# Kernel tuning notes

Hardware: AMD Instinct MI355X
Metric: run time of the kernel (lower is better)

The kernel has to match this reference:

```python
import jax, jax.numpy as jnp
import numpy as np

N_NODES = 50000
N_EDGES = 800000
IN_DIM = 64
EDGE_DIM = 16
HID = 128
L = 3
G = 128  # number of graphs in the batch
EPS = 1e-5


def _glorot(key, shape):
    fan_in, fan_out = shape[0], shape[1]
    lim = float(np.sqrt(6.0 / (fan_in + fan_out)))
    return jax.random.uniform(key, shape, jnp.float32, -lim, lim)


def setup_inputs() -> dict:
    key = jax.random.key(0)
    ks = jax.random.split(key, 40)
    inp = {}
    inp["x"] = jax.random.uniform(ks[0], (N_NODES, IN_DIM), jnp.float32)
    inp["edge_index"] = jax.random.randint(ks[1], (2, N_EDGES), 0, N_NODES, jnp.int64)
    inp["edge_attr"] = jax.random.normal(ks[2], (N_EDGES, EDGE_DIM), jnp.float32)
    inp["batch"] = jnp.sort(jax.random.randint(ks[3], (N_NODES,), 0, G, jnp.int64))
    # ligand / protein input MLPs: Linear-ReLU-Linear-ReLU
    inp["lig_w1"] = _glorot(ks[4], (IN_DIM, HID)); inp["lig_b1"] = jnp.zeros((HID,), jnp.float32)
    inp["lig_w2"] = _glorot(ks[5], (HID, HID));    inp["lig_b2"] = jnp.zeros((HID,), jnp.float32)
    inp["prot_w1"] = _glorot(ks[6], (IN_DIM, HID)); inp["prot_b1"] = jnp.zeros((HID,), jnp.float32)
    inp["prot_w2"] = _glorot(ks[7], (HID, HID));    inp["prot_b2"] = jnp.zeros((HID,), jnp.float32)
    # per-layer GINEConv params (stacked over layers)
    inp["edge_w"] = jnp.stack([_glorot(ks[8 + i], (EDGE_DIM, HID)) for i in range(L)])
    inp["edge_b"] = jnp.zeros((L, HID), jnp.float32)
    inp["nn_w1"] = jnp.stack([_glorot(ks[12 + i], (HID, HID)) for i in range(L)])
    inp["nn_b1"] = jnp.zeros((L, HID), jnp.float32)
    inp["nn_w2"] = jnp.stack([_glorot(ks[16 + i], (HID, HID)) for i in range(L)])
    inp["nn_b2"] = jnp.zeros((L, HID), jnp.float32)
    # GraphNorm params: weight=1, bias=0, mean_scale=1
    inp["gn_w"] = jnp.ones((L, HID), jnp.float32)
    inp["gn_b"] = jnp.zeros((L, HID), jnp.float32)
    inp["gn_ms"] = jnp.ones((L, HID), jnp.float32)
    # output head: Linear-ReLU-Linear(1)
    inp["fc_w1"] = _glorot(ks[20], (HID, HID)); inp["fc_b1"] = jnp.zeros((HID,), jnp.float32)
    inp["fc_w2"] = _glorot(ks[21], (HID, 1));   inp["fc_b2"] = jnp.zeros((1,), jnp.float32)
    return inp


def reference(x, edge_index, edge_attr, batch,
              lig_w1, lig_b1, lig_w2, lig_b2,
              prot_w1, prot_b1, prot_w2, prot_b2,
              edge_w, edge_b, nn_w1, nn_b1, nn_w2, nn_b2,
              gn_w, gn_b, gn_ms,
              fc_w1, fc_b1, fc_w2, fc_b2):
    relu = lambda a: jnp.maximum(a, 0)
    src, dst = edge_index[0], edge_index[1]

    # input encoders, merged per node by protein flag (last feature column)
    is_prot = x[:, -1] > 0.5
    h_lig = relu(relu(x @ lig_w1 + lig_b1) @ lig_w2 + lig_b2)
    h_prot = relu(relu(x @ prot_w1 + prot_b1) @ prot_w2 + prot_b2)
    h = jnp.where(is_prot[:, None], h_prot, h_lig)

    # per-graph node counts for GraphNorm
    cnt = jax.ops.segment_sum(jnp.ones((x.shape[0],), jnp.float32), batch, num_segments=G)
    cnt = jnp.maximum(cnt, 1.0)[:, None]

    for l in range(L):
        # GINEConv (eps=0): out = nn(x + sum_{j->i} relu(x_j + lin(e_ji)))
        e = edge_attr @ edge_w[l] + edge_b[l]              # [E, HID]
        msg = relu(h[src] + e)                             # gather + add + relu
        aggr = jax.ops.segment_sum(msg, dst, num_segments=h.shape[0])
        h = aggr + h
        h = relu(h @ nn_w1[l] + nn_b1[l]) @ nn_w2[l] + nn_b2[l]
        # GraphNorm: per-graph mean/var with learnable mean_scale
        mean = jax.ops.segment_sum(h, batch, num_segments=G) / cnt
        hc = h - mean[batch] * gn_ms[l]
        var = jax.ops.segment_sum(hc * hc, batch, num_segments=G) / cnt
        h = gn_w[l] * hc * jax.lax.rsqrt(var[batch] + EPS) + gn_b[l]
        h = relu(h)  # (dropout=0.0 -> identity)

    g = jax.ops.segment_sum(h, batch, num_segments=G)      # global_add_pool
    out = relu(g @ fc_w1 + fc_b1) @ fc_w2 + fc_b2
    return out.reshape(-1)
```

## Files before the change

### kernel.cpp

```cpp
#include <hip/hip_runtime.h>

#define N_NODES 50000
#define N_EDGES 800000
#define IN_DIM  64
#define EDGE_DIM 16
#define HID     128
#define NLAYERS 3
#define NGRAPH  128
#define EPS     1e-5f

typedef __attribute__((ext_vector_type(8))) short bf8_t;
typedef __attribute__((ext_vector_type(4))) float f32x4;

__device__ __forceinline__ unsigned short f2bf(float x) {
    unsigned u = __float_as_uint(x);
    unsigned r = u + 0x7fffu + ((u >> 16) & 1u);
    return (unsigned short)(r >> 16);
}
__device__ __forceinline__ float bf2f(unsigned short v) {
    return __uint_as_float(((unsigned)v) << 16);
}

__global__ void k_init(int* __restrict__ row_cnt, float* __restrict__ pool,
                       float* __restrict__ gsum, float* __restrict__ gsq) {
    int i = blockIdx.x * blockDim.x + threadIdx.x;
    if (i < N_NODES) row_cnt[i] = 0;
    if (i < NGRAPH * HID) { pool[i] = 0.0f; gsum[i] = 0.0f; gsq[i] = 0.0f; }
}

__global__ __launch_bounds__(NGRAPH) void k_count(const int* __restrict__ batch,
                                                  float* __restrict__ cnt) {
    int g = threadIdx.x;
    int lo = 0, hi = N_NODES;
    while (lo < hi) { int mid = (lo + hi) >> 1; if (batch[mid] < g) lo = mid + 1; else hi = mid; }
    int a = lo;
    lo = 0; hi = N_NODES;
    while (lo < hi) { int mid = (lo + hi) >> 1; if (batch[mid] < g + 1) lo = mid + 1; else hi = mid; }
    cnt[g] = (float)(lo - a);
}

__global__ void k_wconv(const float* __restrict__ nw1, const float* __restrict__ nw2,
                        unsigned short* __restrict__ wt) {
    int idx = blockIdx.x * 256 + threadIdx.x;
    if (idx >= NLAYERS * 2 * HID * HID) return;
    int k = idx & 127;
    int n = (idx >> 7) & 127;
    int which = (idx >> 14) & 1;
    int l = idx >> 15;
    const float* w = (which == 0 ? nw1 : nw2) + l * HID * HID;
    wt[idx] = f2bf(w[k * HID + n]);
}

__global__ void k_wconv_enc(const float* __restrict__ lw1, const float* __restrict__ pw1,
                            const float* __restrict__ lw2, const float* __restrict__ pw2,
                            unsigned short* __restrict__ we) {
    int idx = blockIdx.x * 256 + threadIdx.x;
    if (idx >= 49152) return;
    float v;
    if (idx < 8192)       { int n = idx >> 6, k = idx & 63;            v = lw1[k * HID + n]; }
    else if (idx < 16384) { int r = idx - 8192;  int n = r >> 6, k = r & 63;  v = pw1[k * HID + n]; }
    else if (idx < 32768) { int r = idx - 16384; int n = r >> 7, k = r & 127; v = lw2[k * HID + n]; }
    else                  { int r = idx - 32768; int n = r >> 7, k = r & 127; v = pw2[k * HID + n]; }
    we[idx] = f2bf(v);
}

__global__ void k_wconv_e(const float* __restrict__ ew, unsigned short* __restrict__ wte) {
    int idx = blockIdx.x * 256 + threadIdx.x;
    if (idx >= NLAYERS * 8 * 64 * 8) return;
    int j = idx & 7;
    int lane = (idx >> 3) & 63;
    int t = (idx >> 9) & 7;
    int l = idx >> 12;
    int k = (lane >> 4) * 8 + j;
    int feat = t * 16 + (lane & 15);
    float v = (k < EDGE_DIM) ? ew[l * EDGE_DIM * HID + k * HID + feat] : 0.0f;
    wte[idx] = f2bf(v);
}

__global__ void k_hist(const int* __restrict__ dsts, int* __restrict__ row_cnt) {
    int e = blockIdx.x * blockDim.x + threadIdx.x;
    if (e < N_EDGES) atomicAdd(&row_cnt[dsts[e]], 1);
}

__global__ __launch_bounds__(256) void k_scan1(const int* __restrict__ row_cnt,
                                               int* __restrict__ partial) {
    __shared__ int s[256];
    int t = threadIdx.x, b = blockIdx.x;
    int i0 = b * 512 + t;
    int v = 0;
    if (i0 < N_NODES) v += row_cnt[i0];
    if (i0 + 256 < N_NODES) v += row_cnt[i0 + 256];
    s[t] = v; __syncthreads();
    for (int off = 128; off > 0; off >>= 1) {
        if (t < off) s[t] += s[t + off];
        __syncthreads();
    }
    if (t == 0) partial[b] = s[0];
}

#define NCHUNK 98
__global__ __launch_bounds__(128) void k_scan2(int* __restrict__ partial) {
    __shared__ int s[128];
    int t = threadIdx.x;
    int v = (t < NCHUNK) ? partial[t] : 0;
    s[t] = v; __syncthreads();
    for (int off = 1; off < 128; off <<= 1) {
        int x = (t >= off) ? s[t - off] : 0;
        __syncthreads();
        s[t] += x;
        __syncthreads();
    }
    partial[t] = s[t] - v;
}

__global__ __launch_bounds__(512) void k_scan3(const int* __restrict__ row_cnt,
                                               const int* __restrict__ partial,
                                               int* __restrict__ row_start,
                                               int* __restrict__ row_fill) {
    __shared__ int s[512];
    int t = threadIdx.x, b = blockIdx.x;
    int i = b * 512 + t;
    int v = (i < N_NODES) ? row_cnt[i] : 0;
    s[t] = v; __syncthreads();
    for (int off = 1; off < 512; off <<= 1) {
        int x = (t >= off) ? s[t - off] : 0;
        __syncthreads();
        s[t] += x;
        __syncthreads();
    }
    int excl = s[t] - v + partial[b];
    if (i < N_NODES) { row_start[i] = excl; row_fill[i] = excl; }
}

__global__ void k_fill(const int* __restrict__ srcs, const int* __restrict__ dsts,
                       const float* __restrict__ ea,
                       int* __restrict__ row_fill,
                       int* __restrict__ csr_src, unsigned short* __restrict__ cea) {
    int e = blockIdx.x * blockDim.x + threadIdx.x;
    if (e < N_EDGES) {
        int p = atomicAdd(&row_fill[dsts[e]], 1);
        csr_src[p] = srcs[e];
        const float* s = ea + (size_t)e * EDGE_DIM;
        bf8_t v0, v1;
        #pragma unroll
        for (int k = 0; k < 8; ++k) v0[k] = (short)f2bf(s[k]);
        #pragma unroll
        for (int k = 0; k < 8; ++k) v1[k] = (short)f2bf(s[8 + k]);
        *(bf8_t*)(cea + (size_t)p * EDGE_DIM) = v0;
        *(bf8_t*)(cea + (size_t)p * EDGE_DIM + 8) = v1;
    }
}

#define HS 136
__global__ __launch_bounds__(256) void k_encoder_mfma(
    const float* __restrict__ x,
    const unsigned short* __restrict__ we,
    const float* __restrict__ lb1, const float* __restrict__ lb2,
    const float* __restrict__ pb1, const float* __restrict__ pb2,
    unsigned short* __restrict__ Hbp) {
    __shared__ short h1l[4 * 16 * HS];
    __shared__ short h1p[4 * 16 * HS];
    int w = threadIdx.x >> 6, lane = threadIdx.x & 63;
    int m = lane & 15, quad = lane >> 4;
    int nb = blockIdx.x * 64 + w * 16;
    short* hl = h1l + w * 16 * HS;
    short* hp = h1p + w * 16 * HS;
    int nclamp = nb + m; if (nclamp >= N_NODES) nclamp = N_NODES - 1;
    const float* xp = x + (size_t)nclamp * IN_DIM;

    f32x4 a1l[8], a1p[8];
    #pragma unroll
    for (int t = 0; t < 8; ++t) {
        float bl = lb1[t * 16 + m], bp = pb1[t * 16 + m];
        a1l[t] = (f32x4){bl, bl, bl, bl};
        a1p[t] = (f32x4){bp, bp, bp, bp};
    }
    #pragma unroll
    for (int s_ = 0; s_ < 2; ++s_) {
        int k0 = s_ * 32 + quad * 8;
        float4 a0 = *(const float4*)(xp + k0);
        float4 a1v = *(const float4*)(xp + k0 + 4);
        bf8_t af;
        af[0] = (short)f2bf(a0.x); af[1] = (short)f2bf(a0.y);
        af[2] = (short)f2bf(a0.z); af[3] = (short)f2bf(a0.w);
        af[4] = (short)f2bf(a1v.x); af[5] = (short)f2bf(a1v.y);
        af[6] = (short)f2bf(a1v.z); af[7] = (short)f2bf(a1v.w);
        #pragma unroll
        for (int t = 0; t < 8; ++t) {
            bf8_t bl = *(const bf8_t*)(we + (t * 16 + m) * 64 + k0);
            bf8_t bp = *(const bf8_t*)(we + 8192 + (t * 16 + m) * 64 + k0);
            a1l[t] = __builtin_amdgcn_mfma_f32_16x16x32_bf16(af, bl, a1l[t], 0, 0, 0);
            a1p[t] = __builtin_amdgcn_mfma_f32_16x16x32_bf16(af, bp, a1p[t], 0, 0, 0);
        }
    }
    #pragma unroll
    for (int t = 0; t < 8; ++t)
        #pragma unroll
        for (int r = 0; r < 4; ++r) {
            hl[(quad * 4 + r) * HS + t * 16 + m] = (short)f2bf(fmaxf(a1l[t][r], 0.0f));
            hp[(quad * 4 + r) * HS + t * 16 + m] = (short)f2bf(fmaxf(a1p[t][r], 0.0f));
        }
    __syncthreads();
    f32x4 a2l[8], a2p[8];
    #pragma unroll
    for (int t = 0; t < 8; ++t) {
        float bl = lb2[t * 16 + m], bp = pb2[t * 16 + m];
        a2l[t] = (f32x4){bl, bl, bl, bl};
        a2p[t] = (f32x4){bp, bp, bp, bp};
    }
    #pragma unroll
    for (int s_ = 0; s_ < 4; ++s_) {
        int k0 = s_ * 32 + quad * 8;
        bf8_t afl = *(const bf8_t*)(hl + m * HS + k0);
        bf8_t afp = *(const bf8_t*)(hp + m * HS + k0);
        #pragma unroll
        for (int t = 0; t < 8; ++t) {
            bf8_t bl = *(const bf8_t*)(we + 16384 + (t * 16 + m) * 128 + k0);
            bf8_t bp = *(const bf8_t*)(we + 32768 + (t * 16 + m) * 128 + k0);
            a2l[t] = __builtin_amdgcn_mfma_f32_16x16x32_bf16(afl, bl, a2l[t], 0, 0, 0);
            a2p[t] = __builtin_amdgcn_mfma_f32_16x16x32_bf16(afp, bp, a2p[t], 0, 0, 0);
        }
    }
    #pragma unroll
    for (int r = 0; r < 4; ++r) {
        int node = nb + quad * 4 + r;
        if (node < N_NODES) {
            float flg = x[(size_t)node * IN_DIM + (IN_DIM - 1)];
            bool prot = flg > 0.5f;
            bf8_t o;
            #pragma unroll
            for (int t = 0; t < 8; ++t) {
                float v = prot ? a2p[t][r] : a2l[t][r];
                o[t] = (short)f2bf(fmaxf(v, 0.0f));
            }
            *(bf8_t*)(Hbp + (size_t)node * HID + m * 8) = o;
        }
    }
}

__global__ __launch_bounds__(256) void k_gather(
    const int* __restrict__ csr_src, const unsigned short* __restrict__ cea,
    const int* __restrict__ row_start, const int* __restrict__ row_end,
    const unsigned short* __restrict__ wte, const float* __restrict__ eb,
    const unsigned short* __restrict__ Hbp, float* __restrict__ A) {
    int w = threadIdx.x >> 6, lane = threadIdx.x & 63;
    int m = lane & 15, quad = lane >> 4;
    int n = blockIdx.x * 4 + w;
    bf8_t bw[8];
    #pragma unroll
    for (int t = 0; t < 8; ++t)
        bw[t] = *(const bf8_t*)(wte + ((size_t)t * 64 + lane) * 8);
    float ebv[8];
    #pragma unroll
    for (int t = 0; t < 8; ++t) ebv[t] = eb[t * 16 + m];
    float acc[8];
    #pragma unroll
    for (int t = 0; t < 8; ++t) acc[t] = 0.0f;

    int p  = __builtin_amdgcn_readfirstlane(row_start[n]);
    int pe = __builtin_amdgcn_readfirstlane(row_end[n]);

    for (; p + 16 <= pe; p += 16) {
        bf8_t af = (bf8_t){0, 0, 0, 0, 0, 0, 0, 0};
        if (quad < 2)
            af = *(const bf8_t*)(cea + (size_t)(p + m) * EDGE_DIM + quad * 8);
        int sr[4];
        #pragma unroll
        for (int r = 0; r < 4; ++r) sr[r] = csr_src[p + quad * 4 + r];
        bf8_t hrow[4];
        #pragma unroll
        for (int r = 0; r < 4; ++r)
            hrow[r] = *(const bf8_t*)(Hbp + (size_t)sr[r] * HID + m * 8);
        f32x4 d[8];
        #pragma unroll
        for (int t = 0; t < 8; ++t)
            d[t] = __builtin_amdgcn_mfma_f32_16x16x32_bf16(
                af, bw[t], (f32x4){ebv[t], ebv[t], ebv[t], ebv[t]}, 0, 0, 0);
        #pragma unroll
        for (int t = 0; t < 8; ++t)
            #pragma unroll
            for (int r = 0; r < 4; ++r)
                acc[t] += fmaxf(bf2f((unsigned short)hrow[r][t]) + d[t][r], 0.0f);
    }
    int rem = pe - p;
    if (rem > 0) {
        bf8_t af = (bf8_t){0, 0, 0, 0, 0, 0, 0, 0};
        if (quad < 2 && m < rem)
            af = *(const bf8_t*)(cea + (size_t)(p + m) * EDGE_DIM + quad * 8);
        int sr[4];
        #pragma unroll
        for (int r = 0; r < 4; ++r) {
            int idx = p + quad * 4 + r; if (idx >= pe) idx = pe - 1;
            sr[r] = csr_src[idx];
        }
        bf8_t hrow[4];
        #pragma unroll
        for (int r = 0; r < 4; ++r)
            hrow[r] = *(const bf8_t*)(Hbp + (size_t)sr[r] * HID + m * 8);
        f32x4 d[8];
        #pragma unroll
        for (int t = 0; t < 8; ++t)
            d[t] = __builtin_amdgcn_mfma_f32_16x16x32_bf16(
                af, bw[t], (f32x4){ebv[t], ebv[t], ebv[t], ebv[t]}, 0, 0, 0);
        #pragma unroll
        for (int t = 0; t < 8; ++t)
            #pragma unroll
            for (int r = 0; r < 4; ++r)
                if (quad * 4 + r < rem)
                    acc[t] += fmaxf(bf2f((unsigned short)hrow[r][t]) + d[t][r], 0.0f);
    }
    #pragma unroll
    for (int t = 0; t < 8; ++t) {
        acc[t] += __shfl_xor(acc[t], 16);
        acc[t] += __shfl_xor(acc[t], 32);
    }
    int t0 = quad * 2, t1 = quad * 2 + 1;
    const unsigned short* selfp = Hbp + (size_t)n * HID + m * 8;
    float s0 = bf2f(selfp[t0]);
    float s1 = bf2f(selfp[t1]);
    size_t base = (size_t)n * HID;
    A[base + t0 * 16 + m] = acc[t0] + s0;
    A[base + t1 * 16 + m] = acc[t1] + s1;
}

#define MLP_NODES_PER_BLOCK 64
__global__ __launch_bounds__(256) void k_mlp_mfma(
    const float* __restrict__ A, const int* __restrict__ batch,
    const unsigned short* __restrict__ wt1, const unsigned short* __restrict__ wt2,
    const float* __restrict__ b1, const float* __restrict__ b2,
    float* __restrict__ H, float* __restrict__ gsum, float* __restrict__ gsq) {
    __shared__ short h1s[4 * 16 * HS];
    int w = threadIdx.x >> 6;
    int lane = threadIdx.x & 63;
    int m = lane & 15;
    int quad = lane >> 4;
    int nb = blockIdx.x * MLP_NODES_PER_BLOCK + w * 16;
    short* hw = h1s + w * 16 * HS;

    int nclamp = nb + m; if (nclamp >= N_NODES) nclamp = N_NODES - 1;
    const float* Ap = A + (size_t)nclamp * HID;
    f32x4 acc1[8];
    #pragma unroll
    for (int t = 0; t < 8; ++t) {
        float bv = b1[t * 16 + m];
        acc1[t] = (f32x4){bv, bv, bv, bv};
    }
    #pragma unroll
    for (int s_ = 0; s_ < 4; ++s_) {
        int k0 = s_ * 32 + quad * 8;
        float4 a0 = *(const float4*)(Ap + k0);
        float4 a1 = *(const float4*)(Ap + k0 + 4);
        bf8_t af;
        af[0] = (short)f2bf(a0.x); af[1] = (short)f2bf(a0.y);
        af[2] = (short)f2bf(a0.z); af[3] = (short)f2bf(a0.w);
        af[4] = (short)f2bf(a1.x); af[5] = (short)f2bf(a1.y);
        af[6] = (short)f2bf(a1.z); af[7] = (short)f2bf(a1.w);
        #pragma unroll
        for (int t = 0; t < 8; ++t) {
            bf8_t bf = *(const bf8_t*)(wt1 + (t * 16 + m) * HID + k0);
            acc1[t] = __builtin_amdgcn_mfma_f32_16x16x32_bf16(af, bf, acc1[t], 0, 0, 0);
        }
    }
    #pragma unroll
    for (int t = 0; t < 8; ++t)
        #pragma unroll
        for (int r = 0; r < 4; ++r) {
            float v = fmaxf(acc1[t][r], 0.0f);
            hw[(quad * 4 + r) * HS + t * 16 + m] = (short)f2bf(v);
        }
    __syncthreads();
    f32x4 acc2[8];
    #pragma unroll
    for (int t = 0; t < 8; ++t) {
        float bv = b2[t * 16 + m];
        acc2[t] = (f32x4){bv, bv, bv, bv};
    }
    #pragma unroll
    for (int s_ = 0; s_ < 4; ++s_) {
        int k0 = s_ * 32 + quad * 8;
        bf8_t af = *(const bf8_t*)(hw + m * HS + k0);
        #pragma unroll
        for (int t = 0; t < 8; ++t) {
            bf8_t bf = *(const bf8_t*)(wt2 + (t * 16 + m) * HID + k0);
            acc2[t] = __builtin_amdgcn_mfma_f32_16x16x32_bf16(af, bf, acc2[t], 0, 0, 0);
        }
    }
    #pragma unroll
    for (int t = 0; t < 8; ++t)
        #pragma unroll
        for (int r = 0; r < 4; ++r) {
            int node = nb + quad * 4 + r;
            if (node < N_NODES) H[(size_t)node * HID + t * 16 + m] = acc2[t][r];
        }
    int blast = nb + 15 < N_NODES ? batch[nb + 15] : -1;
    int g0 = batch[nb < N_NODES ? nb : N_NODES - 1];
    if (nb + 15 < N_NODES && g0 == blast) {
        #pragma unroll
        for (int t = 0; t < 8; ++t) {
            float s = 0.0f, q = 0.0f;
            #pragma unroll
            for (int r = 0; r < 4; ++r) { float v = acc2[t][r]; s += v; q += v * v; }
            s += __shfl_xor(s, 16); q += __shfl_xor(q, 16);
            s += __shfl_xor(s, 32); q += __shfl_xor(q, 32);
            if (quad == 0) {
                atomicAdd(&gsum[g0 * HID + t * 16 + m], s);
                atomicAdd(&gsq[g0 * HID + t * 16 + m], q);
            }
        }
    } else {
        #pragma unroll
        for (int t = 0; t < 8; ++t)
            #pragma unroll
            for (int r = 0; r < 4; ++r) {
                int node = nb + quad * 4 + r;
                if (node < N_NODES) {
                    int g = batch[node];
                    float v = acc2[t][r];
                    atomicAdd(&gsum[g * HID + t * 16 + m], v);
                    atomicAdd(&gsq[g * HID + t * 16 + m], v * v);
                }
            }
    }
}

__global__ __launch_bounds__(HID) void k_stats(
    float* __restrict__ gsum, float* __restrict__ gsq,
    const float* __restrict__ cnt,
    const float* __restrict__ gw, const float* __restrict__ gb,
    const float* __restrict__ gms,
    float* __restrict__ sc, float* __restrict__ of) {
    int g = blockIdx.x;
    int t = threadIdx.x;
    float c = fmaxf(cnt[g], 1.0f);
    float mean = gsum[g * HID + t] / c;
    float msq  = gsq[g * HID + t] / c;
    float ms = gms[t];
    float var = msq - mean * mean * ms * (2.0f - ms);
    var = fmaxf(var, 0.0f);
    float istd = rsqrtf(var + EPS);
    float s = gw[t] * istd;
    sc[g * HID + t] = s;
    of[g * HID + t] = gb[t] - s * mean * ms;
    gsum[g * HID + t] = 0.0f;
    gsq[g * HID + t]  = 0.0f;
}

#define NORM_N 8
__global__ __launch_bounds__(HID) void k_norm(
    const float* __restrict__ H, const int* __restrict__ batch,
    const float* __restrict__ sc, const float* __restrict__ of,
    unsigned short* __restrict__ Hbp, float* __restrict__ pool, int accumulate) {
    int n0 = blockIdx.x * NORM_N;
    int t = threadIdx.x;
    int m = t & 15, tt = t >> 4;
    int g0 = batch[n0], gN = batch[n0 + NORM_N - 1];
    if (g0 == gN) {
        float ssc = sc[g0 * HID + t], sof = of[g0 * HID + t];
        float ps = 0.0f;
        #pragma unroll
        for (int i = 0; i < NORM_N; ++i) {
            float v = fmaxf(H[(size_t)(n0 + i) * HID + t] * ssc + sof, 0.0f);
            Hbp[(size_t)(n0 + i) * HID + m * 8 + tt] = f2bf(v);
            ps += v;
        }
        if (accumulate) atomicAdd(&pool[g0 * HID + t], ps);
    } else {
        #pragma unroll
        for (int i = 0; i < NORM_N; ++i) {
            int g = batch[n0 + i];
            float v = fmaxf(H[(size_t)(n0 + i) * HID + t] * sc[g * HID + t] + of[g * HID + t], 0.0f);
            Hbp[(size_t)(n0 + i) * HID + m * 8 + tt] = f2bf(v);
            if (accumulate) atomicAdd(&pool[g * HID + t], v);
        }
    }
}

__global__ __launch_bounds__(HID) void k_head(
    const float* __restrict__ pool,
    const float* __restrict__ fw1, const float* __restrict__ fb1,
    const float* __restrict__ fw2, const float* __restrict__ fb2,
    float* __restrict__ out) {
    __shared__ float ps[HID];
    __shared__ float red[2];
    int g = blockIdx.x;
    int t = threadIdx.x;
    ps[t] = pool[g * HID + t];
    __syncthreads();
    float acc = fb1[t];
    #pragma unroll 4
    for (int k = 0; k < HID; ++k) acc = fmaf(ps[k], fw1[k * HID + t], acc);
    float p = fmaxf(acc, 0.0f) * fw2[t];
    #pragma unroll
    for (int off = 32; off > 0; off >>= 1) p += __shfl_down(p, off, 64);
    if ((t & 63) == 0) red[t >> 6] = p;
    __syncthreads();
    if (t == 0) out[g] = red[0] + red[1] + fb2[0];
}

extern "C" void kernel_launch(void* const* d_in, const int* in_sizes, int n_in,
                              void* d_out, int out_size, void* d_ws, size_t ws_size,
                              hipStream_t stream) {
    const float* x     = (const float*)d_in[0];
    const int*   ei    = (const int*)d_in[1];
    const float* ea    = (const float*)d_in[2];
    const int*   batch = (const int*)d_in[3];
    const float* lw1 = (const float*)d_in[4];
    const float* lb1 = (const float*)d_in[5];
    const float* lw2 = (const float*)d_in[6];
    const float* lb2 = (const float*)d_in[7];
    const float* pw1 = (const float*)d_in[8];
    const float* pb1 = (const float*)d_in[9];
    const float* pw2 = (const float*)d_in[10];
    const float* pb2 = (const float*)d_in[11];
    const float* ew  = (const float*)d_in[12];
    const float* eb  = (const float*)d_in[13];
    const float* nw1 = (const float*)d_in[14];
    const float* nb1 = (const float*)d_in[15];
    const float* nw2 = (const float*)d_in[16];
    const float* nb2 = (const float*)d_in[17];
    const float* gw  = (const float*)d_in[18];
    const float* gb  = (const float*)d_in[19];
    const float* gms = (const float*)d_in[20];
    const float* fw1 = (const float*)d_in[21];
    const float* fb1 = (const float*)d_in[22];
    const float* fw2 = (const float*)d_in[23];
    const float* fb2 = (const float*)d_in[24];
    float* out = (float*)d_out;

    float* ws   = (float*)d_ws;
    float* H    = ws;
    float* A    = H    + (size_t)N_NODES * HID;
    float* gsum = A    + (size_t)N_NODES * HID;
    float* gsq  = gsum + NGRAPH * HID;
    float* sc   = gsq  + NGRAPH * HID;
    float* of   = sc   + NGRAPH * HID;
    float* pool = of   + NGRAPH * HID;
    float* cnt  = pool + NGRAPH * HID;
    int* row_cnt   = (int*)(cnt + NGRAPH);
    int* row_start = row_cnt + N_NODES;
    int* row_fill  = row_start + N_NODES;
    int* partial   = row_fill + N_NODES;
    int* csr_src   = partial + 128;
    unsigned short* cea  = (unsigned short*)(csr_src + N_EDGES);
    unsigned short* wt   = cea + (size_t)N_EDGES * EDGE_DIM;
    unsigned short* wenc = wt + NLAYERS * 2 * HID * HID;
    unsigned short* wte  = wenc + 49152;
    unsigned short* Hbp  = wte + NLAYERS * 8 * 64 * 8;

    const int* srcs = ei;
    const int* dsts = ei + N_EDGES;

    k_init<<<(N_NODES + 255) / 256, 256, 0, stream>>>(row_cnt, pool, gsum, gsq);
    k_count<<<1, NGRAPH, 0, stream>>>(batch, cnt);
    k_wconv<<<(NLAYERS * 2 * HID * HID + 255) / 256, 256, 0, stream>>>(nw1, nw2, wt);
    k_wconv_enc<<<(49152 + 255) / 256, 256, 0, stream>>>(lw1, pw1, lw2, pw2, wenc);
    k_wconv_e<<<(NLAYERS * 8 * 64 * 8 + 255) / 256, 256, 0, stream>>>(ew, wte);
    k_hist<<<(N_EDGES + 255) / 256, 256, 0, stream>>>(dsts, row_cnt);
    k_scan1<<<NCHUNK, 256, 0, stream>>>(row_cnt, partial);
    k_scan2<<<1, 128, 0, stream>>>(partial);
    k_scan3<<<NCHUNK, 512, 0, stream>>>(row_cnt, partial, row_start, row_fill);
    k_fill<<<(N_EDGES + 255) / 256, 256, 0, stream>>>(srcs, dsts, ea, row_fill,
                                                      csr_src, cea);

    k_encoder_mfma<<<(N_NODES + 63) / 64, 256, 0, stream>>>(
        x, wenc, lb1, lb2, pb1, pb2, Hbp);

    int mlp_blocks = (N_NODES + MLP_NODES_PER_BLOCK - 1) / MLP_NODES_PER_BLOCK;
    for (int l = 0; l < NLAYERS; ++l) {
        k_gather<<<N_NODES / 4, 256, 0, stream>>>(
            csr_src, cea, row_start, row_fill,
            wte + (size_t)l * 4096, eb + l * HID, Hbp, A);
        k_mlp_mfma<<<mlp_blocks, 256, 0, stream>>>(
            A, batch,
            wt + (size_t)l * 2 * HID * HID,
            wt + (size_t)l * 2 * HID * HID + HID * HID,
            nb1 + l * HID, nb2 + l * HID, H, gsum, gsq);
        k_stats<<<NGRAPH, HID, 0, stream>>>(gsum, gsq, cnt,
                                            gw + l * HID, gb + l * HID, gms + l * HID,
                                            sc, of);
        k_norm<<<N_NODES / NORM_N, HID, 0, stream>>>(
            H, batch, sc, of, Hbp, pool, (l == NLAYERS - 1) ? 1 : 0);
    }
    k_head<<<NGRAPH, HID, 0, stream>>>(pool, fw1, fb1, fw2, fb2, out);
}
```

Measured before the change: 728.7 us.

## Split gather features across two waves, fold edge bias into MFMA, store bf16 aggregate

```diff
diff --git a/kernel.cpp b/kernel.cpp
--- a/kernel.cpp
+++ b/kernel.cpp
@@ -10,6 +10,7 @@
 #define EPS     1e-5f
 
 typedef __attribute__((ext_vector_type(8))) short bf8_t;
+typedef __attribute__((ext_vector_type(4))) short bf4_t;
 typedef __attribute__((ext_vector_type(4))) float f32x4;
 
 __device__ __forceinline__ unsigned short f2bf(float x) {
@@ -64,7 +65,8 @@
     we[idx] = f2bf(v);
 }
 
-__global__ void k_wconv_e(const float* __restrict__ ew, unsigned short* __restrict__ wte) {
+__global__ void k_wconv_e(const float* __restrict__ ew, const float* __restrict__ eb,
+                          unsigned short* __restrict__ wte) {
     int idx = blockIdx.x * 256 + threadIdx.x;
     if (idx >= NLAYERS * 8 * 64 * 8) return;
     int j = idx & 7;
@@ -73,7 +75,9 @@
     int l = idx >> 12;
     int k = (lane >> 4) * 8 + j;
     int feat = t * 16 + (lane & 15);
-    float v = (k < EDGE_DIM) ? ew[l * EDGE_DIM * HID + k * HID + feat] : 0.0f;
+    float v = 0.0f;
+    if (k < EDGE_DIM)       v = ew[l * EDGE_DIM * HID + k * HID + feat];
+    else if (k == EDGE_DIM) v = eb[l * HID + feat];
     wte[idx] = f2bf(v);
 }
 
@@ -238,46 +242,49 @@
     }
 }
 
-__global__ __launch_bounds__(256) void k_gather(
+__global__ __launch_bounds__(256, 8) void k_gather(
     const int* __restrict__ csr_src, const unsigned short* __restrict__ cea,
     const int* __restrict__ row_start, const int* __restrict__ row_end,
-    const unsigned short* __restrict__ wte, const float* __restrict__ eb,
-    const unsigned short* __restrict__ Hbp, float* __restrict__ A) {
+    const unsigned short* __restrict__ wte,
+    const unsigned short* __restrict__ Hbp, unsigned short* __restrict__ Abp) {
     int w = threadIdx.x >> 6, lane = threadIdx.x & 63;
     int m = lane & 15, quad = lane >> 4;
-    int n = blockIdx.x * 4 + w;
-    bf8_t bw[8];
-    #pragma unroll
-    for (int t = 0; t < 8; ++t)
-        bw[t] = *(const bf8_t*)(wte + ((size_t)t * 64 + lane) * 8);
-    float ebv[8];
-    #pragma unroll
-    for (int t = 0; t < 8; ++t) ebv[t] = eb[t * 16 + m];
-    float acc[8];
-    #pragma unroll
-    for (int t = 0; t < 8; ++t) acc[t] = 0.0f;
+    int n = blockIdx.x * 2 + (w >> 1);
+    int half = w & 1;
+
+    bf8_t bw[4];
+    #pragma unroll
+    for (int t = 0; t < 4; ++t)
+        bw[t] = *(const bf8_t*)(wte + ((size_t)(half * 4 + t) * 64 + lane) * 8);
+
+    float acc[4];
+    #pragma unroll
+    for (int t = 0; t < 4; ++t) acc[t] = 0.0f;
 
     int p  = __builtin_amdgcn_readfirstlane(row_start[n]);
     int pe = __builtin_amdgcn_readfirstlane(row_end[n]);
+
+    const f32x4 zc = (f32x4){0.0f, 0.0f, 0.0f, 0.0f};
 
     for (; p + 16 <= pe; p += 16) {
         bf8_t af = (bf8_t){0, 0, 0, 0, 0, 0, 0, 0};
         if (quad < 2)
             af = *(const bf8_t*)(cea + (size_t)(p + m) * EDGE_DIM + quad * 8);
+        else if (quad == 2)
+            af[0] = (short)0x3F80;
         int sr[4];
         #pragma unroll
         for (int r = 0; r < 4; ++r) sr[r] = csr_src[p + quad * 4 + r];
-        bf8_t hrow[4];
+        bf4_t hrow[4];
         #pragma unroll
         for (int r = 0; r < 4; ++r)
-            hrow[r] = *(const bf8_t*)(Hbp + (size_t)sr[r] * HID + m * 8);
-        f32x4 d[8];
-        #pragma unroll
-        for (int t = 0; t < 8; ++t)
-            d[t] = __builtin_amdgcn_mfma_f32_16x16x32_bf16(
-                af, bw[t], (f32x4){ebv[t], ebv[t], ebv[t], ebv[t]}, 0, 0, 0);
-        #pragma unroll
-        for (int t = 0; t < 8; ++t)
+            hrow[r] = *(const bf4_t*)(Hbp + (size_t)sr[r] * HID + m * 8 + half * 4);
+        f32x4 d[4];
+        #pragma unroll
+        for (int t = 0; t < 4; ++t)
+            d[t] = __builtin_amdgcn_mfma_f32_16x16x32_bf16(af, bw[t], zc, 0, 0, 0);
+        #pragma unroll
+        for (int t = 0; t < 4; ++t)
             #pragma unroll
             for (int r = 0; r < 4; ++r)
                 acc[t] += fmaxf(bf2f((unsigned short)hrow[r][t]) + d[t][r], 0.0f);
@@ -287,45 +294,42 @@
         bf8_t af = (bf8_t){0, 0, 0, 0, 0, 0, 0, 0};
         if (quad < 2 && m < rem)
             af = *(const bf8_t*)(cea + (size_t)(p + m) * EDGE_DIM + quad * 8);
+        else if (quad == 2)
+            af[0] = (short)0x3F80;
         int sr[4];
         #pragma unroll
         for (int r = 0; r < 4; ++r) {
             int idx = p + quad * 4 + r; if (idx >= pe) idx = pe - 1;
             sr[r] = csr_src[idx];
         }
-        bf8_t hrow[4];
+        bf4_t hrow[4];
         #pragma unroll
         for (int r = 0; r < 4; ++r)
-            hrow[r] = *(const bf8_t*)(Hbp + (size_t)sr[r] * HID + m * 8);
-        f32x4 d[8];
-        #pragma unroll
-        for (int t = 0; t < 8; ++t)
-            d[t] = __builtin_amdgcn_mfma_f32_16x16x32_bf16(
-                af, bw[t], (f32x4){ebv[t], ebv[t], ebv[t], ebv[t]}, 0, 0, 0);
-        #pragma unroll
-        for (int t = 0; t < 8; ++t)
+            hrow[r] = *(const bf4_t*)(Hbp + (size_t)sr[r] * HID + m * 8 + half * 4);
+        f32x4 d[4];
+        #pragma unroll
+        for (int t = 0; t < 4; ++t)
+            d[t] = __builtin_amdgcn_mfma_f32_16x16x32_bf16(af, bw[t], zc, 0, 0, 0);
+        #pragma unroll
+        for (int t = 0; t < 4; ++t)
             #pragma unroll
             for (int r = 0; r < 4; ++r)
                 if (quad * 4 + r < rem)
                     acc[t] += fmaxf(bf2f((unsigned short)hrow[r][t]) + d[t][r], 0.0f);
     }
     #pragma unroll
-    for (int t = 0; t < 8; ++t) {
+    for (int t = 0; t < 4; ++t) {
         acc[t] += __shfl_xor(acc[t], 16);
         acc[t] += __shfl_xor(acc[t], 32);
     }
-    int t0 = quad * 2, t1 = quad * 2 + 1;
-    const unsigned short* selfp = Hbp + (size_t)n * HID + m * 8;
-    float s0 = bf2f(selfp[t0]);
-    float s1 = bf2f(selfp[t1]);
-    size_t base = (size_t)n * HID;
-    A[base + t0 * 16 + m] = acc[t0] + s0;
-    A[base + t1 * 16 + m] = acc[t1] + s1;
+    float asel = (quad == 0) ? acc[0] : (quad == 1) ? acc[1] : (quad == 2) ? acc[2] : acc[3];
+    float self_ = bf2f(Hbp[(size_t)n * HID + m * 8 + half * 4 + quad]);
+    Abp[(size_t)n * HID + (half * 4 + quad) * 16 + m] = f2bf(asel + self_);
 }
 
 #define MLP_NODES_PER_BLOCK 64
 __global__ __launch_bounds__(256) void k_mlp_mfma(
-    const float* __restrict__ A, const int* __restrict__ batch,
+    const unsigned short* __restrict__ Abp, const int* __restrict__ batch,
     const unsigned short* __restrict__ wt1, const unsigned short* __restrict__ wt2,
     const float* __restrict__ b1, const float* __restrict__ b2,
     float* __restrict__ H, float* __restrict__ gsum, float* __restrict__ gsq) {
@@ -338,7 +342,7 @@
     short* hw = h1s + w * 16 * HS;
 
     int nclamp = nb + m; if (nclamp >= N_NODES) nclamp = N_NODES - 1;
-    const float* Ap = A + (size_t)nclamp * HID;
+    const unsigned short* Ap = Abp + (size_t)nclamp * HID;
     f32x4 acc1[8];
     #pragma unroll
     for (int t = 0; t < 8; ++t) {
@@ -348,13 +352,7 @@
     #pragma unroll
     for (int s_ = 0; s_ < 4; ++s_) {
         int k0 = s_ * 32 + quad * 8;
-        float4 a0 = *(const float4*)(Ap + k0);
-        float4 a1 = *(const float4*)(Ap + k0 + 4);
-        bf8_t af;
-        af[0] = (short)f2bf(a0.x); af[1] = (short)f2bf(a0.y);
-        af[2] = (short)f2bf(a0.z); af[3] = (short)f2bf(a0.w);
-        af[4] = (short)f2bf(a1.x); af[5] = (short)f2bf(a1.y);
-        af[6] = (short)f2bf(a1.z); af[7] = (short)f2bf(a1.w);
+        bf8_t af = *(const bf8_t*)(Ap + k0);
         #pragma unroll
         for (int t = 0; t < 8; ++t) {
             bf8_t bf = *(const bf8_t*)(wt1 + (t * 16 + m) * HID + k0);
@@ -546,6 +544,7 @@
     unsigned short* wenc = wt + NLAYERS * 2 * HID * HID;
     unsigned short* wte  = wenc + 49152;
     unsigned short* Hbp  = wte + NLAYERS * 8 * 64 * 8;
+    unsigned short* Abp  = (unsigned short*)A;
 
     const int* srcs = ei;
     const int* dsts = ei + N_EDGES;
@@ -554,7 +553,7 @@
     k_count<<<1, NGRAPH, 0, stream>>>(batch, cnt);
     k_wconv<<<(NLAYERS * 2 * HID * HID + 255) / 256, 256, 0, stream>>>(nw1, nw2, wt);
     k_wconv_enc<<<(49152 + 255) / 256, 256, 0, stream>>>(lw1, pw1, lw2, pw2, wenc);
-    k_wconv_e<<<(NLAYERS * 8 * 64 * 8 + 255) / 256, 256, 0, stream>>>(ew, wte);
+    k_wconv_e<<<(NLAYERS * 8 * 64 * 8 + 255) / 256, 256, 0, stream>>>(ew, eb, wte);
     k_hist<<<(N_EDGES + 255) / 256, 256, 0, stream>>>(dsts, row_cnt);
     k_scan1<<<NCHUNK, 256, 0, stream>>>(row_cnt, partial);
     k_scan2<<<1, 128, 0, stream>>>(partial);
@@ -567,11 +566,11 @@
 
     int mlp_blocks = (N_NODES + MLP_NODES_PER_BLOCK - 1) / MLP_NODES_PER_BLOCK;
     for (int l = 0; l < NLAYERS; ++l) {
-        k_gather<<<N_NODES / 4, 256, 0, stream>>>(
+        k_gather<<<N_NODES / 2, 256, 0, stream>>>(
             csr_src, cea, row_start, row_fill,
-            wte + (size_t)l * 4096, eb + l * HID, Hbp, A);
+            wte + (size_t)l * 4096, Hbp, Abp);
         k_mlp_mfma<<<mlp_blocks, 256, 0, stream>>>(
-            A, batch,
+            Abp, batch,
             wt + (size_t)l * 2 * HID * HID,
             wt + (size_t)l * 2 * HID * HID + HID * HID,
             nb1 + l * HID, nb2 + l * HID, H, gsum, gsq);
```

After: 673.6 us. 7.6% less time.
